# Kernel optimization log

Hardware: AMD Instinct MI355X
Metric: run time of the kernel (lower is better)

The kernel has to match this reference:

```python
import jax, jax.numpy as jnp
import numpy as np

N, E, T, R, L = 100000, 800000, 2, 4, 2
DIN, H, C, DOUT = 16, 256, 128, 4
EPS = 1e-5


def hetero_linear(x, node_type, W, b):
    # y[i] = x[i] @ W[node_type[i]] + b[node_type[i]]; small fixed T loop
    out = jnp.zeros((x.shape[0], W.shape[-1]), x.dtype)
    for t in range(W.shape[0]):
        out = out + jnp.where((node_type == t)[:, None], x @ W[t] + b[t], jnp.zeros((), x.dtype))
    return out


def hetero_bn(x, node_type, gamma, beta):
    # per-node-type batch norm (training-mode statistics, biased variance)
    T_ = gamma.shape[0]
    cnt = jax.ops.segment_sum(jnp.ones((x.shape[0],), x.dtype), node_type, num_segments=T_)
    cnt = jnp.maximum(cnt, 1.0)[:, None]
    mean = jax.ops.segment_sum(x, node_type, num_segments=T_) / cnt
    var = jax.ops.segment_sum(x * x, node_type, num_segments=T_) / cnt - mean * mean
    inv = jax.lax.rsqrt(var + EPS)
    return (x - mean[node_type]) * inv[node_type] * gamma[node_type] + beta[node_type]


def rgcn_conv(x, edge_index, edge_type, W, root, bias):
    # RGCNConv with sum aggregation: out_i = x_i @ root + b + sum_{(j->i), r} x_j @ W_r
    src, dst = edge_index[0], edge_index[1]
    hs = jnp.einsum('nd,rdf->rnf', x, W)          # [R, N, C]
    msg = hs[edge_type, src]                       # [E, C] per-edge relation-transformed source feats
    agg = jax.ops.segment_sum(msg, dst, num_segments=x.shape[0])
    return agg + x @ root + bias


def setup_inputs() -> dict:
    key = jax.random.key(0)
    ks = iter(jax.random.split(key, 40))

    def w(shape, fan_in):
        return jax.random.normal(next(ks), shape, jnp.float32) / np.float32(np.sqrt(fan_in))

    inp = {}
    inp['x'] = jax.random.normal(next(ks), (N, DIN), jnp.float32)
    inp['edge_index'] = jax.random.randint(next(ks), (2, E), 0, N)
    inp['node_type'] = jax.random.randint(next(ks), (N,), 0, T)
    inp['edge_type'] = jax.random.randint(next(ks), (E,), 0, R)
    inp['ri_w0'] = w((T, DIN, H), DIN); inp['ri_b0'] = jnp.zeros((T, H))
    inp['ri_g0'] = jnp.ones((T, H)); inp['ri_be0'] = jnp.zeros((T, H))
    inp['ri_w1'] = w((T, H, C), H); inp['ri_b1'] = jnp.zeros((T, C))
    inp['cn_g'] = jnp.ones((L, T, C)); inp['cn_b'] = jnp.zeros((L, T, C))
    inp['rg_w'] = w((L, R, C, C), C); inp['rg_root'] = w((L, C, C), C); inp['rg_bias'] = jnp.zeros((L, C))
    inp['mn_g'] = jnp.ones((L, T, C)); inp['mn_b'] = jnp.zeros((L, T, C))
    inp['mw0'] = w((L, T, C, H), C); inp['mb0'] = jnp.zeros((L, T, H))
    inp['mg0'] = jnp.ones((L, T, H)); inp['mbe0'] = jnp.zeros((L, T, H))
    inp['mw1'] = w((L, T, H, C), H); inp['mb1'] = jnp.zeros((L, T, C))
    inp['ro_w0'] = w((T, C, H), C); inp['ro_b0'] = jnp.zeros((T, H))
    inp['ro_g0'] = jnp.ones((T, H)); inp['ro_be0'] = jnp.zeros((T, H))
    inp['ro_w1'] = w((T, H, DOUT), H); inp['ro_b1'] = jnp.zeros((T, DOUT))
    return inp


def reference(x, edge_index, node_type, edge_type,
              ri_w0, ri_b0, ri_g0, ri_be0, ri_w1, ri_b1,
              cn_g, cn_b, rg_w, rg_root, rg_bias,
              mn_g, mn_b, mw0, mb0, mg0, mbe0, mw1, mb1,
              ro_w0, ro_b0, ro_g0, ro_be0, ro_w1, ro_b1):
    act = jax.nn.leaky_relu  # negative_slope 0.01, as nn.LeakyReLU default
    # readin MLP (plain_last)
    h = hetero_linear(x, node_type, ri_w0, ri_b0)
    h = act(hetero_bn(h, node_type, ri_g0, ri_be0))
    h = hetero_linear(h, node_type, ri_w1, ri_b1)
    # RES+ blocks: Norm -> Act -> Conv -> +res, Norm -> Act -> MLP -> +res (dropout=0)
    for l in range(rg_w.shape[0]):
        y = act(hetero_bn(h, node_type, cn_g[l], cn_b[l]))
        h = h + rgcn_conv(y, edge_index, edge_type, rg_w[l], rg_root[l], rg_bias[l])
        y = act(hetero_bn(h, node_type, mn_g[l], mn_b[l]))
        y = hetero_linear(y, node_type, mw0[l], mb0[l])
        y = act(hetero_bn(y, node_type, mg0[l], mbe0[l]))
        y = hetero_linear(y, node_type, mw1[l], mb1[l])
        h = h + y
    # readout MLP (plain_last)
    h = hetero_linear(h, node_type, ro_w0, ro_b0)
    h = act(hetero_bn(h, node_type, ro_g0, ro_be0))
    return hetero_linear(h, node_type, ro_w1, ro_b1)
```

## Files before the change

### kernel.cpp

```cpp
#include <hip/hip_runtime.h>

#define TT 2
#define RR 4
#define LL 2
#define DIN 16
#define HH 256
#define CC 128
#define DOUT 4
#define EPS 1e-5f
#define NB 32
#define NBG 16

typedef float v4f __attribute__((ext_vector_type(4)));
typedef short bf16x8 __attribute__((ext_vector_type(8)));

__device__ __forceinline__ ushort f2bf(float x) {
    uint u = __float_as_uint(x);
    return (ushort)((u + 0x7fffu + ((u >> 16) & 1u)) >> 16);
}
__device__ __forceinline__ float bf2f(ushort h) { return __uint_as_float(((uint)h) << 16); }
__device__ __forceinline__ int swc(int c) { return c ^ ((c >> 3) & 7); }
__device__ __forceinline__ uint pack2(float x, float y) {
    return (uint)f2bf(x) | ((uint)f2bf(y) << 16);
}

__global__ __launch_bounds__(1024) void k_scan1(const int* __restrict__ in, int* __restrict__ out,
                                                int* __restrict__ part, int n) {
    __shared__ int sm[1024];
    const int tid = threadIdx.x;
    const int i = blockIdx.x * 1024 + tid;
    const int v = (i < n) ? in[i] : 0;
    sm[tid] = v;
    __syncthreads();
    for (int off = 1; off < 1024; off <<= 1) {
        const int u = (tid >= off) ? sm[tid - off] : 0;
        __syncthreads();
        sm[tid] += u;
        __syncthreads();
    }
    if (i < n) out[i] = sm[tid] - v;
    if (tid == 1023) part[blockIdx.x] = sm[1023];
}

__global__ __launch_bounds__(1024) void k_scan2(int* __restrict__ part, int nb) {
    __shared__ int sm[1024];
    const int tid = threadIdx.x;
    const int v = (tid < nb) ? part[tid] : 0;
    sm[tid] = v;
    __syncthreads();
    for (int off = 1; off < 1024; off <<= 1) {
        const int u = (tid >= off) ? sm[tid - off] : 0;
        __syncthreads();
        sm[tid] += u;
        __syncthreads();
    }
    if (tid < nb) part[tid] = sm[tid] - v;
    if (tid == nb - 1) part[nb] = sm[tid];
}

__global__ __launch_bounds__(1024) void k_scan3(int* __restrict__ arr, const int* __restrict__ part,
                                                int n, int nb, int* __restrict__ typeStart,
                                                int* __restrict__ out2) {
    const int i = blockIdx.x * 1024 + threadIdx.x;
    if (i < n) {
        const int v = arr[i] + part[i >> 10];
        arr[i] = v;
        if (out2) out2[i] = v;
    } else if (i == n) {
        const int total = part[nb];
        arr[n] = total;
        if (typeStart) { typeStart[0] = 0; typeStart[1] = n - total; typeStart[2] = n; }
    }
}

__global__ __launch_bounds__(256) void k_build_perm(const int* __restrict__ nt, const int* __restrict__ pscan,
                                                    const int* __restrict__ typeStart, int* __restrict__ perm,
                                                    int* __restrict__ inv, int n) {
    const int i = blockIdx.x * 256 + threadIdx.x;
    if (i >= n) return;
    const int s1 = pscan[i];
    const int pos = nt[i] ? (typeStart[1] + s1) : (i - s1);
    perm[pos] = i;
    inv[i] = pos;
}

__global__ __launch_bounds__(256) void k_deg2(const int* __restrict__ dstv, const int* __restrict__ et,
                                              const int* __restrict__ inv, int* __restrict__ rowp2, int nE) {
    const int e = blockIdx.x * 256 + threadIdx.x;
    if (e < nE) atomicAdd(&rowp2[inv[dstv[e]] * 4 + et[e]], 1);
}

__global__ __launch_bounds__(256) void k_fill2(const int* __restrict__ srcv, const int* __restrict__ dstv,
                                               const int* __restrict__ et, const int* __restrict__ inv,
                                               int* __restrict__ cur, int* __restrict__ csr, int nE) {
    const int e = blockIdx.x * 256 + threadIdx.x;
    if (e < nE) {
        const int pos = atomicAdd(&cur[inv[dstv[e]] * 4 + et[e]], 1);
        csr[pos] = inv[srcv[e]];
    }
}

__global__ __launch_bounds__(256) void k_packall(const float* __restrict__ ri_w1, const float* __restrict__ mw0,
                                                 const float* __restrict__ mw1, const float* __restrict__ ro_w0,
                                                 ushort* __restrict__ p_ri1, ushort* __restrict__ p_mw0,
                                                 ushort* __restrict__ p_mw1, ushort* __restrict__ p_ro0) {
    for (long long idx = (long long)blockIdx.x * 256 + threadIdx.x; idx < 393216;
         idx += (long long)gridDim.x * 256) {
        const float* src; ushort* dst; int K, N; long long lo;
        if (idx < 65536)       { src = ri_w1; dst = p_ri1; K = 256; N = 128; lo = idx; }
        else if (idx < 196608) { src = mw0;   dst = p_mw0; K = 128; N = 256; lo = idx - 65536; }
        else if (idx < 327680) { src = mw1;   dst = p_mw1; K = 256; N = 128; lo = idx - 196608; }
        else                   { src = ro_w0; dst = p_ro0; K = 128; N = 256; lo = idx - 327680; }
        const int kn = K * N;
        const int mat = (int)(lo / kn);
        const int rem = (int)(lo - (long long)mat * kn);
        const int k = rem / N, col = rem % N;
        dst[((size_t)mat * (K / 8) + (k >> 3)) * N * 8 + (size_t)col * 8 + (k & 7)] = f2bf(src[lo]);
    }
}

__global__ __launch_bounds__(256) void k_pack_conv(const float* __restrict__ rgw_all,
                                                   const float* __restrict__ root_all,
                                                   ushort* __restrict__ dst_all) {
    const int idx = blockIdx.x * 256 + threadIdx.x;
    if (idx >= 640 * 128) return;
    const int l = blockIdx.y;
    const float* rgw = rgw_all + (size_t)l * RR * CC * CC;
    const float* root = root_all + (size_t)l * CC * CC;
    ushort* dst = dst_all + (size_t)l * 640 * 128;
    const int k = idx >> 7, col = idx & 127;
    const float v = (k < 512) ? rgw[(((k >> 7) * CC) + (k & 127)) * CC + col]
                              : root[(size_t)(k - 512) * CC + col];
    dst[((size_t)(k >> 3) * CC + col) * 8 + (k & 7)] = f2bf(v);
}

__global__ __launch_bounds__(512) void k_coef(const float* __restrict__ stat, const int* __restrict__ typeStart,
                                              const float* __restrict__ g, const float* __restrict__ be,
                                              float* __restrict__ scale, float* __restrict__ shift, int F) {
    const int tid = threadIdx.x;
    if (tid >= TT * F) return;
    const int t = tid / F;
    float s = 0.f, q = 0.f;
    for (int b = 0; b < NB; ++b) {
        s += stat[(size_t)b * 1024 + tid];
        q += stat[(size_t)b * 1024 + 512 + tid];
    }
    const float cnt = fmaxf((float)(typeStart[t + 1] - typeStart[t]), 1.f);
    const float mean = s / cnt;
    const float var = q / cnt - mean * mean;
    const float sc = g[tid] * rsqrtf(var + EPS);
    scale[tid] = sc;
    shift[tid] = be[tid] - mean * sc;
}

__global__ __launch_bounds__(256) void k_bnact(const float* __restrict__ h, const float* __restrict__ scale,
                                               const float* __restrict__ shift, const int* __restrict__ typeStart,
                                               ushort* __restrict__ y16, int n) {
    const int c0 = typeStart[1];
    const long long total = (long long)n * 32;
    for (long long idx = (long long)blockIdx.x * 256 + threadIdx.x; idx < total;
         idx += (long long)gridDim.x * 256) {
        const int i = (int)(idx >> 5), cq = (int)(idx & 31);
        const int t = (i >= c0) ? 1 : 0;
        const v4f v = *(const v4f*)(h + (size_t)i * CC + cq * 4);
        const v4f sc = *(const v4f*)(scale + t * CC + cq * 4);
        const v4f sf = *(const v4f*)(shift + t * CC + cq * 4);
        float o[4];
#pragma unroll
        for (int j = 0; j < 4; ++j) {
            const float vv = fmaf(v[j], sc[j], sf[j]);
            o[j] = fmaxf(vv, 0.01f * vv);
        }
        uint2 p = make_uint2(pack2(o[0], o[1]), pack2(o[2], o[3]));
        *(uint2*)((uint*)y16 + (size_t)i * 64 + cq * 2) = p;
    }
}

__global__ __launch_bounds__(256) void k_agg4(const ushort* __restrict__ y16, const int* __restrict__ rowp2,
                                              const int* __restrict__ csr, ushort* __restrict__ buf,
                                              int q0, int q1) {
    const int wid = threadIdx.x >> 6, lane = threadIdx.x & 63;
    const int i = q0 + blockIdx.x * 4 + wid;
    if (i >= q1) return;
    const uint* y32 = (const uint*)y16;
    float2 a0 = {0.f, 0.f}, a1 = {0.f, 0.f}, a2 = {0.f, 0.f}, a3 = {0.f, 0.f};
    const int e0 = rowp2[4 * i], b1 = rowp2[4 * i + 1], b2 = rowp2[4 * i + 2],
              b3 = rowp2[4 * i + 3], e1 = rowp2[4 * i + 4];
    for (int e = e0; e < e1; e += 64) {
        const int cnt = min(64, e1 - e);
        int pk = (lane < cnt) ? csr[e + lane] : 0;
        for (int j = 0; j < cnt; ++j) {
            const int s = __shfl(pk, j);
            const uint u = y32[(size_t)s * 64 + lane];
            const float vx = bf2f((ushort)(u & 0xffff));
            const float vy = bf2f((ushort)(u >> 16));
            const int idx = e + j;
            if (idx < b1)      { a0.x += vx; a0.y += vy; }
            else if (idx < b2) { a1.x += vx; a1.y += vy; }
            else if (idx < b3) { a2.x += vx; a2.y += vy; }
            else               { a3.x += vx; a3.y += vy; }
        }
    }
    uint* brow = (uint*)buf + (size_t)(i - q0) * 256;
    __builtin_nontemporal_store(pack2(a0.x, a0.y), brow + 0 * 64 + lane);
    __builtin_nontemporal_store(pack2(a1.x, a1.y), brow + 1 * 64 + lane);
    __builtin_nontemporal_store(pack2(a2.x, a2.y), brow + 2 * 64 + lane);
    __builtin_nontemporal_store(pack2(a3.x, a3.y), brow + 3 * 64 + lane);
}

__global__ __launch_bounds__(256) void k_gram(const float* __restrict__ x, const int* __restrict__ perm,
                                              const int* __restrict__ typeStart, float* __restrict__ gram) {
    __shared__ float Xs[256][17];
    const int tid = threadIdx.x;
    const int t = blockIdx.y;
    const int rbeg = typeStart[t], rend = typeStart[t + 1];
    const int r0 = rbeg + blockIdx.x * 1024;
    if (r0 >= rend) return;
    const int i = tid >> 4, j = tid & 15;
    float acc = 0.f, sacc = 0.f;
    for (int rr = 0; rr < 4; ++rr) {
        const int gr = r0 + rr * 256 + tid;
        v4f x0 = 0.f, x1 = 0.f, x2 = 0.f, x3 = 0.f;
        if (gr < rend) {
            const float* xr = x + (size_t)perm[gr] * DIN;
            x0 = *(const v4f*)xr; x1 = *(const v4f*)(xr + 4);
            x2 = *(const v4f*)(xr + 8); x3 = *(const v4f*)(xr + 12);
        }
        __syncthreads();
#pragma unroll
        for (int e = 0; e < 4; ++e) { Xs[tid][e] = x0[e]; Xs[tid][4 + e] = x1[e];
                                      Xs[tid][8 + e] = x2[e]; Xs[tid][12 + e] = x3[e]; }
        __syncthreads();
        for (int r = 0; r < 256; ++r) acc += Xs[r][i] * Xs[r][j];
        if (tid < 16)
            for (int r = 0; r < 256; ++r) sacc += Xs[r][tid];
        __syncthreads();
    }
    float* gb = gram + ((size_t)t * NBG + (blockIdx.x & (NBG - 1))) * 272;
    atomicAdd(&gb[tid], acc);
    if (tid < 16) atomicAdd(&gb[256 + tid], sacc);
}

__global__ __launch_bounds__(512) void k_ri_coef(const float* __restrict__ gram, const int* __restrict__ typeStart,
                                                 const float* __restrict__ ri_w0, const float* __restrict__ ri_b0,
                                                 const float* __restrict__ g, const float* __restrict__ be,
                                                 float* __restrict__ w0eff, float* __restrict__ b0eff) {
    __shared__ float G[2][272];
    const int tid = threadIdx.x;
    for (int idx = tid; idx < 2 * 272; idx += 512) {
        const int tt = idx / 272, k = idx % 272;
        float s = 0.f;
        for (int b = 0; b < NBG; ++b) s += gram[((size_t)tt * NBG + b) * 272 + k];
        G[tt][k] = s;
    }
    __syncthreads();
    const int t = tid >> 8, c = tid & 255;
    float wv[16];
#pragma unroll
    for (int k = 0; k < 16; ++k) wv[k] = ri_w0[((size_t)t * 16 + k) * HH + c];
    const float b = ri_b0[t * HH + c];
    const float cnt = fmaxf((float)(typeStart[t + 1] - typeStart[t]), 1.f);
    float sw = 0.f;
#pragma unroll
    for (int k = 0; k < 16; ++k) sw += G[t][256 + k] * wv[k];
    const float mean = (sw + cnt * b) / cnt;
    float e2 = 0.f;
#pragma unroll
    for (int i = 0; i < 16; ++i) {
        const float wi = wv[i];
#pragma unroll
        for (int j = 0; j < 16; ++j) e2 += wi * wv[j] * G[t][i * 16 + j];
    }
    e2 = (e2 + 2.f * b * sw + cnt * b * b) / cnt;
    const float var = e2 - mean * mean;
    const float sc = g[t * HH + c] * rsqrtf(var + EPS);
    const float sf = be[t * HH + c] - mean * sc;
    b0eff[t * HH + c] = b * sc + sf;
#pragma unroll
    for (int k = 0; k < 16; ++k) w0eff[((size_t)t * 16 + k) * HH + c] = wv[k] * sc;
}

__global__ __launch_bounds__(256) void k_readin(const float* __restrict__ x, const int* __restrict__ perm,
                                                const int* __restrict__ typeStart,
                                                const float* __restrict__ w0eff, const float* __restrict__ b0eff,
                                                const ushort* __restrict__ Wp, const float* __restrict__ b1,
                                                float* __restrict__ h, ushort* __restrict__ h16,
                                                float* __restrict__ stat) {
    __shared__ float Xs[128][17];
    __shared__ float W0s[16][256];
    __shared__ float b0s[256];
    __shared__ ushort As[128][40];
    __shared__ ushort Ws[4][128][8];

    const int tid = threadIdx.x;
    const int lane = tid & 63;
    const int wid = tid >> 6;
    const int woffm = (wid >> 1) * 64, woffn = (wid & 1) * 64;
    const int t = blockIdx.y;
    const int rbeg = typeStart[t], rend = typeStart[t + 1];
    const int r0 = rbeg + blockIdx.x * 128;
    if (r0 >= rend) return;

    for (int idx = tid; idx < 16 * 256; idx += 256) W0s[idx >> 8][idx & 255] = w0eff[(size_t)t * 4096 + idx];
    if (tid < 256) b0s[tid] = b0eff[t * 256 + tid];

    const int srow = tid >> 1, half = tid & 1;
    const int sgr = r0 + srow;
    const bool svalid = sgr < rend;
    {
        v4f x0 = 0.f, x1 = 0.f;
        if (svalid) {
            const float* xr = x + (size_t)perm[sgr] * DIN + half * 8;
            x0 = *(const v4f*)xr; x1 = *(const v4f*)(xr + 4);
        }
#pragma unroll
        for (int e = 0; e < 4; ++e) { Xs[srow][half * 8 + e] = x0[e]; Xs[srow][half * 8 + 4 + e] = x1[e]; }
    }
    __syncthreads();
    float xr[16];
#pragma unroll
    for (int k = 0; k < 16; ++k) xr[k] = Xs[srow][k];

    v4f acc[4][4];
#pragma unroll
    for (int mt = 0; mt < 4; ++mt)
#pragma unroll
        for (int nt = 0; nt < 4; ++nt) acc[mt][nt] = (v4f){0.f, 0.f, 0.f, 0.f};

    const size_t wmat = (size_t)t * 256 * 128;
    const int wcp = tid & 63;

    for (int kt = 0; kt < 8; ++kt) {
        const int k0 = kt * 32;
        ushort hA[16];
#pragma unroll
        for (int c2 = 0; c2 < 16; ++c2) {
            const int col = k0 + half * 16 + c2;
            float d = b0s[col];
#pragma unroll
            for (int k = 0; k < 16; ++k) d = fmaf(xr[k], W0s[k][col], d);
            d = fmaxf(d, 0.01f * d);
            hA[c2] = f2bf(d);
        }
        const ushort* wsrc = Wp + wmat + ((size_t)(k0 / 8 + wid) * 128) * 8 + (size_t)wcp * 16;
        const uint4 w0 = *(const uint4*)wsrc;
        const uint4 w1 = *(const uint4*)(wsrc + 8);
        __syncthreads();
        *(uint4*)&As[srow][half * 16] = *(uint4*)&hA[0];
        *(uint4*)&As[srow][half * 16 + 8] = *(uint4*)&hA[8];
        *(uint4*)&Ws[wid][swc(wcp * 2)][0] = w0;
        *(uint4*)&Ws[wid][swc(wcp * 2 + 1)][0] = w1;
        __syncthreads();
        const int afr = lane & 15;
        const int akg = (lane >> 4) * 8;
        bf16x8 aF[4], wf[4];
#pragma unroll
        for (int mt = 0; mt < 4; ++mt) aF[mt] = *(const bf16x8*)&As[woffm + mt * 16 + afr][akg];
#pragma unroll
        for (int nt = 0; nt < 4; ++nt) wf[nt] = *(const bf16x8*)&Ws[lane >> 4][swc(woffn + nt * 16 + afr)][0];
#pragma unroll
        for (int mt = 0; mt < 4; ++mt)
#pragma unroll
            for (int nt = 0; nt < 4; ++nt)
                acc[mt][nt] = __builtin_amdgcn_mfma_f32_16x16x32_bf16(aF[mt], wf[nt], acc[mt][nt], 0, 0, 0);
    }

    float bv[4];
#pragma unroll
    for (int nt = 0; nt < 4; ++nt) bv[nt] = b1[t * 128 + woffn + nt * 16 + (lane & 15)];
    float cs[4] = {0.f, 0.f, 0.f, 0.f}, cq[4] = {0.f, 0.f, 0.f, 0.f};
#pragma unroll
    for (int mt = 0; mt < 4; ++mt) {
        const int grow = r0 + woffm + mt * 16 + (lane >> 4) * 4;
#pragma unroll
        for (int nt = 0; nt < 4; ++nt) {
            const int gcol = woffn + nt * 16 + (lane & 15);
#pragma unroll
            for (int rg = 0; rg < 4; ++rg) {
                const int gr = grow + rg;
                if (gr < rend) {
                    const float v = acc[mt][nt][rg] + bv[nt];
                    const size_t o = (size_t)gr * 128 + gcol;
                    h[o] = v;
                    h16[o] = f2bf(v);
                    cs[nt] += v; cq[nt] += v * v;
                }
            }
        }
    }
    float* sb = stat + (size_t)(blockIdx.x & (NB - 1)) * 1024;
#pragma unroll
    for (int nt = 0; nt < 4; ++nt) {
        float s = cs[nt], q = cq[nt];
        s += __shfl_xor(s, 16); q += __shfl_xor(q, 16);
        s += __shfl_xor(s, 32); q += __shfl_xor(q, 32);
        if (lane < 16) {
            const int col = t * 128 + woffn + nt * 16 + lane;
            atomicAdd(&sb[col], s);
            atomicAdd(&sb[512 + col], q);
        }
    }
}

template <int K, int OUTW, bool TYPED, bool WHET, bool CROOT, bool BNIN,
          bool BHET, bool STATS, int OUTMODE>
__global__ __launch_bounds__(256) void k_mf(
    const ushort* __restrict__ Xb, const ushort* __restrict__ Xb2,
    const ushort* __restrict__ Wp, const float* __restrict__ Bb,
    const float* __restrict__ scale, const float* __restrict__ shift,
    const int* __restrict__ typeStart, float* __restrict__ Y,
    ushort* __restrict__ Y16, float* __restrict__ stat,
    int rbase, int rbeg_u, int rend_u) {
    constexpr int NT = K / 32;
    constexpr int XSTR = CROOT ? 512 : K;

    __shared__ ushort As[2][64][40];
    __shared__ ushort Ws[2][4][128][8];
    __shared__ float csh[BNIN ? K : 1];
    __shared__ float cfh[BNIN ? K : 1];

    const int tid = threadIdx.x;
    const int lane = tid & 63;
    const int wid = tid >> 6;
    const int kgrp = lane >> 4, fr = lane & 15;
    const int woffm = (wid >> 1) * 32;
    const int woffn = (wid & 1) * 64;

    int t = 0, rbeg = rbeg_u, rend = rend_u;
    if constexpr (TYPED) { t = blockIdx.y; rbeg = typeStart[t]; rend = typeStart[t + 1]; }
    const int r0 = rbeg + blockIdx.x * 64;
    if (r0 >= rend) return;
    const int zoff = (OUTW == 256) ? blockIdx.z * 128 : 0;

    if constexpr (BNIN) {
        for (int k = tid; k < K; k += 256) { csh[k] = scale[t * K + k]; cfh[k] = shift[t * K + k]; }
        __syncthreads();
    }

    const int srow = tid >> 2, skq = tid & 3;
    const int sgr = r0 + srow;
    const bool sv = sgr < rend;
    const int wcp = tid & 63;
    const size_t wmat = (size_t)(WHET ? t : 0) * K * OUTW;

    auto LOADA = [&](int kt) -> uint4 {
        const int k0 = kt * 32;
        uint4 a = make_uint4(0, 0, 0, 0);
        if (sv) {
            const ushort* p;
            if constexpr (CROOT) {
                p = (k0 >= 512) ? (Xb2 + (size_t)sgr * 128 + (k0 - 512) + skq * 8)
                                : (Xb + (size_t)(sgr - rbase) * XSTR + k0 + skq * 8);
            } else {
                p = Xb + (size_t)(sgr - rbase) * XSTR + k0 + skq * 8;
            }
            a = *(const uint4*)p;
        }
        if constexpr (BNIN) {
            uint ua[4] = {a.x, a.y, a.z, a.w};
#pragma unroll
            for (int e = 0; e < 4; ++e) {
                const int k = kt * 32 + skq * 8 + 2 * e;
                float f0 = fmaf(bf2f((ushort)(ua[e] & 0xffff)), csh[k], cfh[k]);
                float f1 = fmaf(bf2f((ushort)(ua[e] >> 16)), csh[k + 1], cfh[k + 1]);
                f0 = fmaxf(f0, 0.01f * f0);
                f1 = fmaxf(f1, 0.01f * f1);
                ua[e] = pack2(f0, f1);
            }
            a = make_uint4(ua[0], ua[1], ua[2], ua[3]);
        }
        return a;
    };
    auto LOADW = [&](int kt, uint4& w0, uint4& w1) {
        const ushort* wsrc = Wp + wmat + ((size_t)(kt * 4 + wid) * OUTW + zoff) * 8 + (size_t)wcp * 16;
        w0 = *(const uint4*)wsrc;
        w1 = *(const uint4*)(wsrc + 8);
    };
    auto STORE = [&](int b, const uint4& a, const uint4& w0, const uint4& w1) {
        *(uint4*)&As[b][srow][skq * 8] = a;
        *(uint4*)&Ws[b][wid][swc(wcp * 2)][0] = w0;
        *(uint4*)&Ws[b][wid][swc(wcp * 2 + 1)][0] = w1;
    };

    v4f acc[2][4];
#pragma unroll
    for (int mt = 0; mt < 2; ++mt)
#pragma unroll
        for (int nt = 0; nt < 4; ++nt) acc[mt][nt] = (v4f){0.f, 0.f, 0.f, 0.f};

    {
        uint4 a = LOADA(0), w0, w1;
        LOADW(0, w0, w1);
        STORE(0, a, w0, w1);
    }
    __syncthreads();

    for (int kt = 0; kt < NT; ++kt) {
        const int cur = kt & 1;
        uint4 na, nw0, nw1;
        const bool more = (kt + 1) < NT;
        if (more) { na = LOADA(kt + 1); LOADW(kt + 1, nw0, nw1); }

        const bf16x8 aF0 = *(const bf16x8*)&As[cur][woffm + fr][kgrp * 8];
        const bf16x8 aF1 = *(const bf16x8*)&As[cur][woffm + 16 + fr][kgrp * 8];
        bf16x8 wf[4];
#pragma unroll
        for (int nt = 0; nt < 4; ++nt)
            wf[nt] = *(const bf16x8*)&Ws[cur][kgrp][swc(woffn + nt * 16 + fr)][0];
#pragma unroll
        for (int nt = 0; nt < 4; ++nt) {
            acc[0][nt] = __builtin_amdgcn_mfma_f32_16x16x32_bf16(aF0, wf[nt], acc[0][nt], 0, 0, 0);
            acc[1][nt] = __builtin_amdgcn_mfma_f32_16x16x32_bf16(aF1, wf[nt], acc[1][nt], 0, 0, 0);
        }
        if (more) {
            STORE(cur ^ 1, na, nw0, nw1);
            __syncthreads();
        }
    }

    const float* BbT = Bb + (BHET ? (size_t)t * OUTW : 0);
    float bv[4];
#pragma unroll
    for (int nt = 0; nt < 4; ++nt) bv[nt] = BbT[zoff + woffn + nt * 16 + fr];
    const int c0 = (STATS && !TYPED) ? typeStart[1] : 0;
    float cs0[4] = {0.f, 0.f, 0.f, 0.f}, cq0[4] = {0.f, 0.f, 0.f, 0.f};
    float cs1[4] = {0.f, 0.f, 0.f, 0.f}, cq1[4] = {0.f, 0.f, 0.f, 0.f};
#pragma unroll
    for (int mt = 0; mt < 2; ++mt) {
        const int grow = r0 + woffm + mt * 16 + kgrp * 4;
#pragma unroll
        for (int nt = 0; nt < 4; ++nt) {
            const int gcol = zoff + woffn + nt * 16 + fr;
#pragma unroll
            for (int rg = 0; rg < 4; ++rg) {
                const int gr = grow + rg;
                if (gr < rend) {
                    float v = acc[mt][nt][rg] + bv[nt];
                    const size_t o = (size_t)gr * OUTW + gcol;
                    if constexpr (OUTMODE == 0) Y[o] = v;
                    if constexpr (OUTMODE == 1) Y16[o] = f2bf(v);
                    if constexpr (OUTMODE == 2) {
                        const float hv = Y[o] + v;
                        Y[o] = hv;
                        Y16[o] = f2bf(hv);
                        v = hv;
                    }
                    if constexpr (STATS) {
                        if (TYPED || gr < c0) { cs0[nt] += v; cq0[nt] += v * v; }
                        else                  { cs1[nt] += v; cq1[nt] += v * v; }
                    }
                }
            }
        }
    }
    if constexpr (STATS) {
        float* sb = stat + (size_t)(blockIdx.x & (NB - 1)) * 1024;
#pragma unroll
        for (int nt = 0; nt < 4; ++nt) {
            float s = cs0[nt], q = cq0[nt];
            s += __shfl_xor(s, 16); q += __shfl_xor(q, 16);
            s += __shfl_xor(s, 32); q += __shfl_xor(q, 32);
            if (lane < 16) {
                const int col = t * OUTW + zoff + woffn + nt * 16 + lane;
                atomicAdd(&sb[col], s);
                atomicAdd(&sb[512 + col], q);
            }
            if constexpr (!TYPED) {
                float s1 = cs1[nt], q1 = cq1[nt];
                s1 += __shfl_xor(s1, 16); q1 += __shfl_xor(q1, 16);
                s1 += __shfl_xor(s1, 32); q1 += __shfl_xor(q1, 32);
                if (lane < 16) {
                    const int col = OUTW + zoff + woffn + nt * 16 + lane;
                    atomicAdd(&sb[col], s1);
                    atomicAdd(&sb[512 + col], q1);
                }
            }
        }
    }
}

__global__ __launch_bounds__(256) void k_ro1(const ushort* __restrict__ A256b, const int* __restrict__ perm,
                                             const int* __restrict__ typeStart, const float* __restrict__ ro_w1,
                                             const float* __restrict__ ro_b1, const float* __restrict__ scale,
                                             const float* __restrict__ shift, float* __restrict__ out, int n) {
    __shared__ float W1s[2][256][4];
    __shared__ float scs[512];
    __shared__ float sfs[512];
    const int tid = threadIdx.x;
    for (int idx = tid; idx < 2048; idx += 256) {
        const int t = idx >> 10, rem = idx & 1023;
        W1s[t][rem >> 2][rem & 3] = ro_w1[idx];
    }
    for (int idx = tid; idx < 512; idx += 256) { scs[idx] = scale[idx]; sfs[idx] = shift[idx]; }
    __syncthreads();
    const int trow = tid >> 2, sub = tid & 3;
    const int gr = blockIdx.x * 64 + trow;
    if (gr >= n) return;
    const int c0 = typeStart[1];
    const int t = (gr >= c0) ? 1 : 0;
    v4f acc = 0.f;
    const ushort* ar = A256b + (size_t)gr * 256 + sub * 64;
#pragma unroll
    for (int q = 0; q < 8; ++q) {
        const uint4 u = *(const uint4*)(ar + q * 8);
        const uint uw[4] = {u.x, u.y, u.z, u.w};
#pragma unroll
        for (int e = 0; e < 4; ++e) {
#pragma unroll
            for (int hl = 0; hl < 2; ++hl) {
                const int col = sub * 64 + q * 8 + 2 * e + hl;
                const float v = bf2f((ushort)(hl ? (uw[e] >> 16) : (uw[e] & 0xffff)));
                float vv = fmaf(v, scs[t * 256 + col], sfs[t * 256 + col]);
                vv = fmaxf(vv, 0.01f * vv);
                acc += vv * *(const v4f*)&W1s[t][col][0];
            }
        }
    }
#pragma unroll
    for (int e = 0; e < 4; ++e) { acc[e] += __shfl_xor(acc[e], 1); acc[e] += __shfl_xor(acc[e], 2); }
    if (sub == 0) {
        acc += *(const v4f*)(ro_b1 + t * 4);
        *(v4f*)(out + (size_t)perm[gr] * 4) = acc;
    }
}

extern "C" void kernel_launch(void* const* d_in, const int* in_sizes, int n_in,
                              void* d_out, int out_size, void* d_ws, size_t ws_size,
                              hipStream_t stream) {
    const float* x = (const float*)d_in[0];
    const int* ei = (const int*)d_in[1];
    const int* nt = (const int*)d_in[2];
    const int* et = (const int*)d_in[3];
    const float* ri_w0 = (const float*)d_in[4];
    const float* ri_b0 = (const float*)d_in[5];
    const float* ri_g0 = (const float*)d_in[6];
    const float* ri_be0 = (const float*)d_in[7];
    const float* ri_w1 = (const float*)d_in[8];
    const float* ri_b1 = (const float*)d_in[9];
    const float* cn_g = (const float*)d_in[10];
    const float* cn_b = (const float*)d_in[11];
    const float* rg_w = (const float*)d_in[12];
    const float* rg_root = (const float*)d_in[13];
    const float* rg_bias = (const float*)d_in[14];
    const float* mn_g = (const float*)d_in[15];
    const float* mn_b = (const float*)d_in[16];
    const float* mw0 = (const float*)d_in[17];
    const float* mb0 = (const float*)d_in[18];
    const float* mg0 = (const float*)d_in[19];
    const float* mbe0 = (const float*)d_in[20];
    const float* mw1 = (const float*)d_in[21];
    const float* mb1 = (const float*)d_in[22];
    const float* ro_w0 = (const float*)d_in[23];
    const float* ro_b0 = (const float*)d_in[24];
    const float* ro_g0 = (const float*)d_in[25];
    const float* ro_be0 = (const float*)d_in[26];
    const float* ro_w1 = (const float*)d_in[27];
    const float* ro_b1 = (const float*)d_in[28];

    const int n = in_sizes[2];
    const int nE = in_sizes[3];
    const int* srcv = ei;
    const int* dstv = ei + nE;

    char* w = (char*)d_ws;
    size_t off = 0;
    auto alloc = [&](size_t bytes) -> char* {
        char* p = w + off;
        off = (off + bytes + 255) & ~(size_t)255;
        return p;
    };
    float* h = (float*)alloc((size_t)n * CC * sizeof(float));
    ushort* h16 = (ushort*)alloc((size_t)(n + 128) * CC * sizeof(ushort));
    int* csr = (int*)alloc((size_t)nE * sizeof(int));
    int* rowp2 = (int*)alloc(((size_t)4 * n + 1) * sizeof(int));
    int* cur2 = (int*)alloc((size_t)4 * n * sizeof(int));
    int* perm = (int*)alloc((size_t)n * sizeof(int));
    int* inv = (int*)alloc((size_t)n * sizeof(int));
    int* pscan = (int*)alloc((size_t)(n + 1) * sizeof(int));
    int* part = (int*)alloc(2052 * sizeof(int));
    int* typeStart = (int*)alloc(64);
    float* statgram = (float*)alloc(((size_t)9 * NB * 1024 + 2 * NBG * 272) * sizeof(float));
    float* scale = (float*)alloc(512 * sizeof(float));
    float* shift = (float*)alloc(512 * sizeof(float));
    float* w0eff = (float*)alloc((size_t)2 * 16 * 256 * sizeof(float));
    float* b0eff = (float*)alloc(512 * sizeof(float));
    ushort* pw_ri1 = (ushort*)alloc(65536 * 2);
    ushort* pw_mw0 = (ushort*)alloc(131072 * 2);
    ushort* pw_mw1 = (ushort*)alloc(131072 * 2);
    ushort* pw_ro0 = (ushort*)alloc(65536 * 2);
    ushort* pw_conv = (ushort*)alloc(163840 * 2);
    char* region2 = alloc((size_t)(n + 128) * 512);
    if (ws_size < off) return;

    float* statbuf = statgram;
    float* gram = statgram + (size_t)9 * NB * 1024;
    ushort* A256b = (ushort*)region2;
    ushort* y16 = (ushort*)region2;
    float* out = (float*)d_out;

    ushort* buf = (ushort*)(w + off);
    const size_t bufBytes = (ws_size > off) ? (ws_size - off) : 0;
    const long long chkcap = (long long)(bufBytes / 1024) - 128;
    if (chkcap < 1024) return;
    int nchunk, CHK;
    if (chkcap >= n) { nchunk = 1; CHK = n; }
    else { nchunk = (int)((n + chkcap - 1) / chkcap); CHK = (n + nchunk - 1) / nchunk; }

    auto SS = [&](int slot) { return statbuf + (size_t)slot * NB * 1024; };

    const int gE = (nE + 255) / 256;
    const int gN = (n + 255) / 256;
    const int nb = (n + 1023) / 1024;
    const int m4 = 4 * n;
    const int nb2 = (m4 + 1023) / 1024;
    const int gmx = (n + 127) / 128;
    const int gm64 = (n + 63) / 64;

    k_packall<<<1536, 256, 0, stream>>>(ri_w1, mw0, mw1, ro_w0, pw_ri1, pw_mw0, pw_mw1, pw_ro0);
    k_pack_conv<<<dim3(320, 2), 256, 0, stream>>>(rg_w, rg_root, pw_conv);

    hipMemsetAsync(statgram, 0, ((size_t)9 * NB * 1024 + 2 * NBG * 272) * sizeof(float), stream);
    k_scan1<<<nb, 1024, 0, stream>>>(nt, pscan, part, n);
    k_scan2<<<1, 1024, 0, stream>>>(part, nb);
    k_scan3<<<(n + 1024) / 1024, 1024, 0, stream>>>(pscan, part, n, nb, typeStart, nullptr);
    k_build_perm<<<gN, 256, 0, stream>>>(nt, pscan, typeStart, perm, inv, n);
    hipMemsetAsync(rowp2, 0, ((size_t)m4 + 1) * sizeof(int), stream);
    k_deg2<<<gE, 256, 0, stream>>>(dstv, et, inv, rowp2, nE);
    k_scan1<<<nb2, 1024, 0, stream>>>(rowp2, rowp2, part, m4);
    k_scan2<<<1, 1024, 0, stream>>>(part, nb2);
    k_scan3<<<(m4 + 1024) / 1024, 1024, 0, stream>>>(rowp2, part, m4, nb2, nullptr, cur2);
    k_fill2<<<gE, 256, 0, stream>>>(srcv, dstv, et, inv, cur2, csr, nE);

    k_gram<<<dim3((n + 1023) / 1024, 2), 256, 0, stream>>>(x, perm, typeStart, gram);
    k_ri_coef<<<1, 512, 0, stream>>>(gram, typeStart, ri_w0, ri_b0, ri_g0, ri_be0, w0eff, b0eff);
    k_readin<<<dim3(gmx, 2), 256, 0, stream>>>(x, perm, typeStart, w0eff, b0eff, pw_ri1, ri_b1,
                                               h, h16, SS(1));

    for (int l = 0; l < LL; ++l) {
        const int s_cn = l ? 4 : 1, s_mn = l ? 5 : 2, s_mg = l ? 6 : 3, s_nx = l ? 7 : 4;
        k_coef<<<1, 512, 0, stream>>>(SS(s_cn), typeStart, cn_g + (size_t)l * TT * CC,
                                      cn_b + (size_t)l * TT * CC, scale, shift, CC);
        k_bnact<<<4096, 256, 0, stream>>>(h, scale, shift, typeStart, y16, n);
        const ushort* wconv = pw_conv + (size_t)l * 640 * 128;
        for (int q0 = 0; q0 < n; q0 += CHK) {
            const int q1 = min(n, q0 + CHK);
            k_agg4<<<(q1 - q0 + 3) / 4, 256, 0, stream>>>(y16, rowp2, csr, buf, q0, q1);
            k_mf<640, 128, false, false, true, false, false, true, 2>
                <<<(q1 - q0 + 63) / 64, 256, 0, stream>>>(
                    buf, y16, wconv, rg_bias + (size_t)l * CC, nullptr, nullptr,
                    typeStart, h, h16, SS(s_mn), q0, q0, q1);
        }

        k_coef<<<1, 512, 0, stream>>>(SS(s_mn), typeStart, mn_g + (size_t)l * TT * CC,
                                      mn_b + (size_t)l * TT * CC, scale, shift, CC);
        k_mf<128, 256, true, true, false, true, true, true, 1><<<dim3(gm64, 2, 2), 256, 0, stream>>>(
            h16, nullptr, pw_mw0 + (size_t)l * 2 * 128 * 256, mb0 + (size_t)l * TT * HH,
            scale, shift, typeStart, nullptr, A256b, SS(s_mg), 0, 0, n);
        k_coef<<<1, 512, 0, stream>>>(SS(s_mg), typeStart, mg0 + (size_t)l * TT * HH,
                                      mbe0 + (size_t)l * TT * HH, scale, shift, HH);
        if (l == 0)
            k_mf<256, 128, true, true, false, true, true, true, 2><<<dim3(gm64, 2, 1), 256, 0, stream>>>(
                A256b, nullptr, pw_mw1 + (size_t)l * 2 * 256 * 128, mb1 + (size_t)l * TT * CC,
                scale, shift, typeStart, h, h16, SS(s_nx), 0, 0, n);
        else
            k_mf<256, 128, true, true, false, true, true, false, 2><<<dim3(gm64, 2, 1), 256, 0, stream>>>(
                A256b, nullptr, pw_mw1 + (size_t)l * 2 * 256 * 128, mb1 + (size_t)l * TT * CC,
                scale, shift, typeStart, h, h16, nullptr, 0, 0, n);
    }

    k_mf<128, 256, true, true, false, false, true, true, 1><<<dim3(gm64, 2, 2), 256, 0, stream>>>(
        h16, nullptr, pw_ro0, ro_b0, nullptr, nullptr, typeStart, nullptr, A256b, SS(8), 0, 0, n);
    k_coef<<<1, 512, 0, stream>>>(SS(8), typeStart, ro_g0, ro_be0, scale, shift, HH);
    k_ro1<<<(n + 63) / 64, 256, 0, stream>>>(A256b, perm, typeStart, ro_w1, ro_b1, scale, shift, out, n);
}
```

Baseline: 725.1 us.

## Fold BN coefficient reduction into consumers and deepen GEMM load pipeline

Removes the separate single-block k_coef launches before the BN-activation kernel and the MLP GEMMs. Each consuming block now reduces the partial statistics and computes scale/shift into shared memory itself. The k_mf main loop is restructured into an unrolled two-stage prefetch that keeps two k-tiles of loads in flight in registers. It also swaps nontemporal stores in k_agg4 for normal stores and cuts the k_bnact grid. Every block now redundantly does the NB-way stat reduction and the GEMM uses more registers, which may lower occupancy.

```diff
diff --git a/kernel.cpp b/kernel.cpp
--- a/kernel.cpp
+++ b/kernel.cpp
@@ -153,22 +153,39 @@
     shift[tid] = be[tid] - mean * sc;
 }
 
-__global__ __launch_bounds__(256) void k_bnact(const float* __restrict__ h, const float* __restrict__ scale,
-                                               const float* __restrict__ shift, const int* __restrict__ typeStart,
+__global__ __launch_bounds__(256) void k_bnact(const float* __restrict__ h, const float* __restrict__ stat_in,
+                                               const float* __restrict__ gg, const float* __restrict__ bb,
+                                               const int* __restrict__ typeStart,
                                                ushort* __restrict__ y16, int n) {
+    __shared__ float scs[2 * CC];
+    __shared__ float sfs[2 * CC];
+    const int tid = threadIdx.x;
+    for (int idx = tid; idx < 2 * CC; idx += 256) {
+        const int t = idx >> 7;
+        float s = 0.f, q = 0.f;
+        for (int b = 0; b < NB; ++b) {
+            s += stat_in[(size_t)b * 1024 + idx];
+            q += stat_in[(size_t)b * 1024 + 512 + idx];
+        }
+        const float cnt = fmaxf((float)(typeStart[t + 1] - typeStart[t]), 1.f);
+        const float mean = s / cnt;
+        const float var = q / cnt - mean * mean;
+        const float sc = gg[idx] * rsqrtf(var + EPS);
+        scs[idx] = sc;
+        sfs[idx] = bb[idx] - mean * sc;
+    }
+    __syncthreads();
     const int c0 = typeStart[1];
     const long long total = (long long)n * 32;
     for (long long idx = (long long)blockIdx.x * 256 + threadIdx.x; idx < total;
          idx += (long long)gridDim.x * 256) {
         const int i = (int)(idx >> 5), cq = (int)(idx & 31);
-        const int t = (i >= c0) ? 1 : 0;
+        const int tb = (i >= c0) ? CC : 0;
         const v4f v = *(const v4f*)(h + (size_t)i * CC + cq * 4);
-        const v4f sc = *(const v4f*)(scale + t * CC + cq * 4);
-        const v4f sf = *(const v4f*)(shift + t * CC + cq * 4);
         float o[4];
 #pragma unroll
         for (int j = 0; j < 4; ++j) {
-            const float vv = fmaf(v[j], sc[j], sf[j]);
+            const float vv = fmaf(v[j], scs[tb + cq * 4 + j], sfs[tb + cq * 4 + j]);
             o[j] = fmaxf(vv, 0.01f * vv);
         }
         uint2 p = make_uint2(pack2(o[0], o[1]), pack2(o[2], o[3]));
@@ -202,10 +219,10 @@
         }
     }
     uint* brow = (uint*)buf + (size_t)(i - q0) * 256;
-    __builtin_nontemporal_store(pack2(a0.x, a0.y), brow + 0 * 64 + lane);
-    __builtin_nontemporal_store(pack2(a1.x, a1.y), brow + 1 * 64 + lane);
-    __builtin_nontemporal_store(pack2(a2.x, a2.y), brow + 2 * 64 + lane);
-    __builtin_nontemporal_store(pack2(a3.x, a3.y), brow + 3 * 64 + lane);
+    brow[0 * 64 + lane] = pack2(a0.x, a0.y);
+    brow[1 * 64 + lane] = pack2(a1.x, a1.y);
+    brow[2 * 64 + lane] = pack2(a2.x, a2.y);
+    brow[3 * 64 + lane] = pack2(a3.x, a3.y);
 }
 
 __global__ __launch_bounds__(256) void k_gram(const float* __restrict__ x, const int* __restrict__ perm,
@@ -407,9 +424,9 @@
 __global__ __launch_bounds__(256) void k_mf(
     const ushort* __restrict__ Xb, const ushort* __restrict__ Xb2,
     const ushort* __restrict__ Wp, const float* __restrict__ Bb,
-    const float* __restrict__ scale, const float* __restrict__ shift,
-    const int* __restrict__ typeStart, float* __restrict__ Y,
-    ushort* __restrict__ Y16, float* __restrict__ stat,
+    const float* __restrict__ stat_in, const float* __restrict__ gg,
+    const float* __restrict__ bb, const int* __restrict__ typeStart,
+    float* __restrict__ Y, ushort* __restrict__ Y16, float* __restrict__ stat,
     int rbase, int rbeg_u, int rend_u) {
     constexpr int NT = K / 32;
     constexpr int XSTR = CROOT ? 512 : K;
@@ -433,7 +450,19 @@
     const int zoff = (OUTW == 256) ? blockIdx.z * 128 : 0;
 
     if constexpr (BNIN) {
-        for (int k = tid; k < K; k += 256) { csh[k] = scale[t * K + k]; cfh[k] = shift[t * K + k]; }
+        const float cnt = fmaxf((float)(typeStart[t + 1] - typeStart[t]), 1.f);
+        for (int k = tid; k < K; k += 256) {
+            float s = 0.f, q = 0.f;
+            for (int b = 0; b < NB; ++b) {
+                s += stat_in[(size_t)b * 1024 + t * K + k];
+                q += stat_in[(size_t)b * 1024 + 512 + t * K + k];
+            }
+            const float mean = s / cnt;
+            const float var = q / cnt - mean * mean;
+            const float sc = gg[t * K + k] * rsqrtf(var + EPS);
+            csh[k] = sc;
+            cfh[k] = bb[t * K + k] - mean * sc;
+        }
         __syncthreads();
     }
 
@@ -488,32 +517,43 @@
 #pragma unroll
         for (int nt = 0; nt < 4; ++nt) acc[mt][nt] = (v4f){0.f, 0.f, 0.f, 0.f};
 
-    {
-        uint4 a = LOADA(0), w0, w1;
-        LOADW(0, w0, w1);
-        STORE(0, a, w0, w1);
-    }
-    __syncthreads();
-
-    for (int kt = 0; kt < NT; ++kt) {
-        const int cur = kt & 1;
-        uint4 na, nw0, nw1;
-        const bool more = (kt + 1) < NT;
-        if (more) { na = LOADA(kt + 1); LOADW(kt + 1, nw0, nw1); }
-
-        const bf16x8 aF0 = *(const bf16x8*)&As[cur][woffm + fr][kgrp * 8];
-        const bf16x8 aF1 = *(const bf16x8*)&As[cur][woffm + 16 + fr][kgrp * 8];
+    auto MSTEP = [&](int b) {
+        const bf16x8 aF0 = *(const bf16x8*)&As[b][woffm + fr][kgrp * 8];
+        const bf16x8 aF1 = *(const bf16x8*)&As[b][woffm + 16 + fr][kgrp * 8];
         bf16x8 wf[4];
 #pragma unroll
         for (int nt = 0; nt < 4; ++nt)
-            wf[nt] = *(const bf16x8*)&Ws[cur][kgrp][swc(woffn + nt * 16 + fr)][0];
+            wf[nt] = *(const bf16x8*)&Ws[b][kgrp][swc(woffn + nt * 16 + fr)][0];
 #pragma unroll
         for (int nt = 0; nt < 4; ++nt) {
             acc[0][nt] = __builtin_amdgcn_mfma_f32_16x16x32_bf16(aF0, wf[nt], acc[0][nt], 0, 0, 0);
             acc[1][nt] = __builtin_amdgcn_mfma_f32_16x16x32_bf16(aF1, wf[nt], acc[1][nt], 0, 0, 0);
         }
-        if (more) {
-            STORE(cur ^ 1, na, nw0, nw1);
+    };
+
+    uint4 aA = make_uint4(0, 0, 0, 0), wA0 = aA, wA1 = aA;
+    uint4 aB = aA, wB0 = aA, wB1 = aA;
+    {
+        uint4 a0 = LOADA(0), w0, w1;
+        LOADW(0, w0, w1);
+        STORE(0, a0, w0, w1);
+    }
+    if (NT > 1) { aA = LOADA(1); LOADW(1, wA0, wA1); }
+    if (NT > 2) { aB = LOADA(2); LOADW(2, wB0, wB1); }
+    __syncthreads();
+
+#pragma unroll
+    for (int kt = 0; kt < NT; kt += 2) {
+        MSTEP(0);
+        {
+            STORE(1, aA, wA0, wA1);
+            if (kt + 3 < NT) { aA = LOADA(kt + 3); LOADW(kt + 3, wA0, wA1); }
+            __syncthreads();
+        }
+        MSTEP(1);
+        if (kt + 2 < NT) {
+            STORE(0, aB, wB0, wB1);
+            if (kt + 4 < NT) { aB = LOADA(kt + 4); LOADW(kt + 4, wB0, wB1); }
             __syncthreads();
         }
     }
@@ -738,38 +778,36 @@
 
     for (int l = 0; l < LL; ++l) {
         const int s_cn = l ? 4 : 1, s_mn = l ? 5 : 2, s_mg = l ? 6 : 3, s_nx = l ? 7 : 4;
-        k_coef<<<1, 512, 0, stream>>>(SS(s_cn), typeStart, cn_g + (size_t)l * TT * CC,
-                                      cn_b + (size_t)l * TT * CC, scale, shift, CC);
-        k_bnact<<<4096, 256, 0, stream>>>(h, scale, shift, typeStart, y16, n);
+        k_bnact<<<1280, 256, 0, stream>>>(h, SS(s_cn), cn_g + (size_t)l * TT * CC,
+                                          cn_b + (size_t)l * TT * CC, typeStart, y16, n);
         const ushort* wconv = pw_conv + (size_t)l * 640 * 128;
         for (int q0 = 0; q0 < n; q0 += CHK) {
             const int q1 = min(n, q0 + CHK);
             k_agg4<<<(q1 - q0 + 3) / 4, 256, 0, stream>>>(y16, rowp2, csr, buf, q0, q1);
             k_mf<640, 128, false, false, true, false, false, true, 2>
                 <<<(q1 - q0 + 63) / 64, 256, 0, stream>>>(
-                    buf, y16, wconv, rg_bias + (size_t)l * CC, nullptr, nullptr,
+                    buf, y16, wconv, rg_bias + (size_t)l * CC, nullptr, nullptr, nullptr,
                     typeStart, h, h16, SS(s_mn), q0, q0, q1);
         }
 
-        k_coef<<<1, 512, 0, stream>>>(SS(s_mn), typeStart, mn_g + (size_t)l * TT * CC,
-                                      mn_b + (size_t)l * TT * CC, scale, shift, CC);
         k_mf<128, 256, true, true, false, true, true, true, 1><<<dim3(gm64, 2, 2), 256, 0, stream>>>(
             h16, nullptr, pw_mw0 + (size_t)l * 2 * 128 * 256, mb0 + (size_t)l * TT * HH,
-            scale, shift, typeStart, nullptr, A256b, SS(s_mg), 0, 0, n);
-        k_coef<<<1, 512, 0, stream>>>(SS(s_mg), typeStart, mg0 + (size_t)l * TT * HH,
-                                      mbe0 + (size_t)l * TT * HH, scale, shift, HH);
+            SS(s_mn), mn_g + (size_t)l * TT * CC, mn_b + (size_t)l * TT * CC,
+            typeStart, nullptr, A256b, SS(s_mg), 0, 0, n);
         if (l == 0)
             k_mf<256, 128, true, true, false, true, true, true, 2><<<dim3(gm64, 2, 1), 256, 0, stream>>>(
                 A256b, nullptr, pw_mw1 + (size_t)l * 2 * 256 * 128, mb1 + (size_t)l * TT * CC,
-                scale, shift, typeStart, h, h16, SS(s_nx), 0, 0, n);
+                SS(s_mg), mg0 + (size_t)l * TT * HH, mbe0 + (size_t)l * TT * HH,
+                typeStart, h, h16, SS(s_nx), 0, 0, n);
         else
             k_mf<256, 128, true, true, false, true, true, false, 2><<<dim3(gm64, 2, 1), 256, 0, stream>>>(
                 A256b, nullptr, pw_mw1 + (size_t)l * 2 * 256 * 128, mb1 + (size_t)l * TT * CC,
-                scale, shift, typeStart, h, h16, nullptr, 0, 0, n);
+                SS(s_mg), mg0 + (size_t)l * TT * HH, mbe0 + (size_t)l * TT * HH,
+                typeStart, h, h16, nullptr, 0, 0, n);
     }
 
     k_mf<128, 256, true, true, false, false, true, true, 1><<<dim3(gm64, 2, 2), 256, 0, stream>>>(
-        h16, nullptr, pw_ro0, ro_b0, nullptr, nullptr, typeStart, nullptr, A256b, SS(8), 0, 0, n);
+        h16, nullptr, pw_ro0, ro_b0, nullptr, nullptr, nullptr, typeStart, nullptr, A256b, SS(8), 0, 0, n);
     k_coef<<<1, 512, 0, stream>>>(SS(8), typeStart, ro_g0, ro_be0, scale, shift, HH);
     k_ro1<<<(n + 63) / 64, 256, 0, stream>>>(A256b, perm, typeStart, ro_w1, ro_b1, scale, shift, out, n);
 }
```

Result: no change. 712.4 us (-1.7%).
